# Performance work log

Hardware: AMD Instinct MI355X
Metric: run time of the kernel (lower is better)

## Reference

```python
import jax, jax.numpy as jnp
import numpy as np

N_NODES = 50000
N_EDGES = 800000
IN_CH = 128
OUT_CH = 64
BN_EPS = 1e-5


def setup_inputs() -> dict:
    key = jax.random.key(0)
    k1, k2, k3 = jax.random.split(key, 3)
    x = jax.random.normal(k1, (N_NODES, IN_CH), dtype=jnp.float32)
    edge_index = jax.random.randint(k2, (2, N_EDGES), 0, N_NODES, dtype=jnp.int64)
    W = jax.random.normal(k3, (IN_CH, OUT_CH), dtype=jnp.float32) / np.sqrt(IN_CH)
    bias = jnp.zeros((OUT_CH,), dtype=jnp.float32)
    gamma = jnp.ones((OUT_CH,), dtype=jnp.float32)
    beta = jnp.zeros((OUT_CH,), dtype=jnp.float32)
    return {"x": x, "edge_index": edge_index, "W": W, "bias": bias,
            "gamma": gamma, "beta": beta}


def reference(x, edge_index, W, bias, gamma, beta):
    N = x.shape[0]
    # Linear transform first (GCNConv order): [N, out]
    h = x @ W
    # Add self-loops
    loops = jnp.arange(N, dtype=edge_index.dtype)
    src = jnp.concatenate([edge_index[0], loops])  # [E+N]
    dst = jnp.concatenate([edge_index[1], loops])
    # Symmetric GCN normalization: deg^{-1/2}[src] * deg^{-1/2}[dst]
    ones = jnp.ones(dst.shape[0], dtype=h.dtype)
    deg = jax.ops.segment_sum(ones, dst, num_segments=N)
    dinv = jnp.where(deg > 0, jax.lax.rsqrt(deg), 0.0)
    norm = dinv[src] * dinv[dst]  # [E+N]
    # Gather, scale, scatter-add
    msgs = h[src] * norm[:, None]  # [E+N, out]
    agg = jax.ops.segment_sum(msgs, dst, num_segments=N) + bias  # [N, out]
    # tanh activation
    a = jnp.tanh(agg)
    # BatchNorm over node dim (training mode, biased var)
    mean = jnp.mean(a, axis=0)
    var = jnp.mean(jnp.square(a - mean), axis=0)
    return gamma * (a - mean) * jax.lax.rsqrt(var + BN_EPS) + beta
```

## Files before the change

kernel.cpp:

```cpp
#include <hip/hip_runtime.h>
#include <hip/hip_bf16.h>
#include <math.h>

#define N_NODES 50000
#define N_EDGES 800000
#define IN_CH 128
#define OUT_CH 64
#define BN_EPS 1e-5f
#define CAP 64

typedef __attribute__((ext_vector_type(8))) short short8;
typedef __attribute__((ext_vector_type(4))) float f32x4;

__device__ __forceinline__ float bf16u_to_f32(uint u) { return __uint_as_float(u << 16); }

__device__ __forceinline__ ushort f32_to_bf16(float f) {
    uint u = __float_as_uint(f);
    uint r = (u + 0x7fff + ((u >> 16) & 1)) >> 16;
    return (ushort)r;
}

__global__ void fill_slots_kernel(const int2* __restrict__ esrc2, const int2* __restrict__ edst2,
                                  int* __restrict__ cnt, ushort* __restrict__ slot, int E2) {
    int i = blockIdx.x * blockDim.x + threadIdx.x;
    if (i < E2) {
        int2 s = esrc2[i];
        int2 d = edst2[i];
        int p0 = atomicAdd(&cnt[d.x], 1);
        int p1 = atomicAdd(&cnt[d.y], 1);
        if (p0 < CAP) slot[d.x * CAP + p0] = (ushort)s.x;
        if (p1 < CAP) slot[d.y * CAP + p1] = (ushort)s.y;
    }
}

#define XPAD 136
__global__ __launch_bounds__(256) void gemm_mfma_kernel(const float* __restrict__ x,
                                                        const float* __restrict__ W,
                                                        const int* __restrict__ cnt,
                                                        ushort* __restrict__ hb,
                                                        float* __restrict__ dinv, int N) {
    __shared__ ushort xs[64 * XPAD];
    __shared__ ushort wt[64 * XPAD];
    int t = threadIdx.x;
    int lane = t & 63;
    int w = t >> 6;
    int nn = lane & 15;
    int quad = lane >> 4;
    int row0 = blockIdx.x * 64;

    const float4* W4 = (const float4*)W;
#pragma unroll
    for (int i = 0; i < 8; ++i) {
        int f4 = t + 256 * i;
        float4 v = W4[f4];
        int e0 = f4 * 4;
        int k = e0 >> 6;
        int n = e0 & 63;
        wt[(n + 0) * XPAD + k] = f32_to_bf16(v.x);
        wt[(n + 1) * XPAD + k] = f32_to_bf16(v.y);
        wt[(n + 2) * XPAD + k] = f32_to_bf16(v.z);
        wt[(n + 3) * XPAD + k] = f32_to_bf16(v.w);
    }
#pragma unroll
    for (int i = 0; i < 8; ++i) {
        int linear4 = t + 256 * i;
        int r = linear4 >> 5;
        int c4 = linear4 & 31;
        int gr = row0 + r; if (gr >= N) gr = N - 1;
        float4 v = *(const float4*)(x + (size_t)gr * IN_CH + c4 * 4);
        ushort u0 = f32_to_bf16(v.x), u1 = f32_to_bf16(v.y);
        ushort u2 = f32_to_bf16(v.z), u3 = f32_to_bf16(v.w);
        uint2 packed = make_uint2((uint)u0 | ((uint)u1 << 16), (uint)u2 | ((uint)u3 << 16));
        *(uint2*)&xs[r * XPAD + c4 * 4] = packed;
    }
    __syncthreads();

    short8 bfrag[4][4];
#pragma unroll
    for (int t2 = 0; t2 < 4; ++t2)
#pragma unroll
        for (int c = 0; c < 4; ++c)
            bfrag[t2][c] = *(const short8*)&wt[(16 * t2 + nn) * XPAD + 32 * c + quad * 8];

    f32x4 acc[4] = {{0.f, 0.f, 0.f, 0.f}, {0.f, 0.f, 0.f, 0.f},
                    {0.f, 0.f, 0.f, 0.f}, {0.f, 0.f, 0.f, 0.f}};
#pragma unroll
    for (int c = 0; c < 4; ++c) {
        short8 afrag = *(const short8*)&xs[(16 * w + nn) * XPAD + 32 * c + quad * 8];
#pragma unroll
        for (int t2 = 0; t2 < 4; ++t2)
            acc[t2] = __builtin_amdgcn_mfma_f32_16x16x32_bf16(afrag, bfrag[t2][c], acc[t2], 0, 0, 0);
    }

    int rbase = row0 + 16 * w + quad * 4;
    float dv[4];
#pragma unroll
    for (int r = 0; r < 4; ++r)
        dv[r] = (rbase + r < N) ? rsqrtf((float)(cnt[rbase + r] + 1)) : 0.f;
    if (nn == 0) {
#pragma unroll
        for (int r = 0; r < 4; ++r)
            if (rbase + r < N) dinv[rbase + r] = dv[r];
    }
#pragma unroll
    for (int t2 = 0; t2 < 4; ++t2) {
#pragma unroll
        for (int r = 0; r < 4; ++r) {
            int row = rbase + r;
            if (row < N) hb[(size_t)row * OUT_CH + 16 * t2 + nn] = f32_to_bf16(acc[t2][r] * dv[r]);
        }
    }
}

__device__ __forceinline__ float reduce_groups(float a0, float a1, float a2, float a3,
                                               float a4, float a5, float a6, float a7, int g) {
    float s0 = a0 + __shfl_xor(a0, 8);
    float s1 = a1 + __shfl_xor(a1, 8);
    float s2 = a2 + __shfl_xor(a2, 8);
    float s3 = a3 + __shfl_xor(a3, 8);
    float s4 = a4 + __shfl_xor(a4, 8);
    float s5 = a5 + __shfl_xor(a5, 8);
    float s6 = a6 + __shfl_xor(a6, 8);
    float s7 = a7 + __shfl_xor(a7, 8);
    bool h1 = (g & 1);
    float b0 = h1 ? s4 : s0, b1 = h1 ? s5 : s1, b2 = h1 ? s6 : s2, b3 = h1 ? s7 : s3;
    float u0 = b0 + __shfl_xor(b0, 16);
    float u1 = b1 + __shfl_xor(b1, 16);
    float u2 = b2 + __shfl_xor(b2, 16);
    float u3 = b3 + __shfl_xor(b3, 16);
    bool h2 = (g & 2);
    float c0 = h2 ? u2 : u0, c1 = h2 ? u3 : u1;
    float v0 = c0 + __shfl_xor(c0, 32);
    float v1 = c1 + __shfl_xor(c1, 32);
    return (g & 4) ? v1 : v0;
}

__global__ __launch_bounds__(256) void gather_fused_kernel(const int* __restrict__ cnt,
                                                           const ushort* __restrict__ slot,
                                                           const float* __restrict__ dinv,
                                                           const ushort* __restrict__ hb,
                                                           const float* __restrict__ bias,
                                                           float* __restrict__ out,
                                                           float* __restrict__ sums, int N) {
    int t = threadIdx.x;
    int lane = t & 63;
    int g = lane >> 3;
    int sub = lane & 7;
    int cidx = 8 * sub + (((g & 1) << 2) | (g & 2) | ((g >> 2) & 1));
    int wid = (blockIdx.x * blockDim.x + t) >> 6;
    int nw = (gridDim.x * blockDim.x) >> 6;
    float bias_c = bias[cidx];
    float ssum = 0.f, ssq = 0.f;

#define ISSUE(SV, MM, DN, J, H0, H1) do {                                  \
        int e0 = (J) + g, e1 = e0 + 8;                                     \
        int i0 = e0 - 1; i0 = (i0 < 0) ? 0 : i0;                           \
        int s0 = __shfl(SV, i0);                                           \
        int s1 = __shfl(SV, e1 - 1);                                       \
        s0 = (e0 == 0) ? (DN) : s0;                                        \
        s0 = (e0 < (MM)) ? s0 : N_NODES;                                   \
        s1 = (e1 < (MM)) ? s1 : N_NODES;                                   \
        H0 = *(const uint4*)(hb + ((size_t)s0 << 6) + (sub << 3));         \
        H1 = *(const uint4*)(hb + ((size_t)s1 << 6) + (sub << 3));         \
    } while (0)

#define CONS_A(H)                                                           \
        aA0 += __uint_as_float((H).x << 16); aA1 += __uint_as_float((H).x & 0xffff0000u); \
        aA2 += __uint_as_float((H).y << 16); aA3 += __uint_as_float((H).y & 0xffff0000u); \
        aA4 += __uint_as_float((H).z << 16); aA5 += __uint_as_float((H).z & 0xffff0000u); \
        aA6 += __uint_as_float((H).w << 16); aA7 += __uint_as_float((H).w & 0xffff0000u);

#define CONS_B(H)                                                           \
        aB0 += __uint_as_float((H).x << 16); aB1 += __uint_as_float((H).x & 0xffff0000u); \
        aB2 += __uint_as_float((H).y << 16); aB3 += __uint_as_float((H).y & 0xffff0000u); \
        aB4 += __uint_as_float((H).z << 16); aB5 += __uint_as_float((H).z & 0xffff0000u); \
        aB6 += __uint_as_float((H).w << 16); aB7 += __uint_as_float((H).w & 0xffff0000u);

    for (int dA = wid; dA < N; dA += 2 * nw) {
        int dB = dA + nw;
        bool hasB = dB < N;
        int dBc = hasB ? dB : dA;

        float ddA = dinv[dA];
        float ddB = dinv[dBc];
        int mA = cnt[dA]; if (mA > CAP) mA = CAP;
        int mB = cnt[dBc]; if (mB > CAP) mB = CAP;
        int svA = __builtin_nontemporal_load(&slot[(size_t)dA * CAP + lane]);
        int svB = __builtin_nontemporal_load(&slot[(size_t)dBc * CAP + lane]);
        int MA = mA + 1;
        int MB = hasB ? mB + 1 : 0;
        int Mmax = (MA > MB) ? MA : MB;

        float aA0 = 0.f, aA1 = 0.f, aA2 = 0.f, aA3 = 0.f;
        float aA4 = 0.f, aA5 = 0.f, aA6 = 0.f, aA7 = 0.f;
        float aB0 = 0.f, aB1 = 0.f, aB2 = 0.f, aB3 = 0.f;
        float aB4 = 0.f, aB5 = 0.f, aB6 = 0.f, aB7 = 0.f;

        uint4 hA0, hA1, hB0, hB1;
        ISSUE(svA, MA, dA, 0, hA0, hA1);
        ISSUE(svB, MB, dBc, 0, hB0, hB1);
        for (int j = 16; j < Mmax; j += 16) {
            uint4 nA0, nA1, nB0, nB1;
            ISSUE(svA, MA, dA, j, nA0, nA1);
            ISSUE(svB, MB, dBc, j, nB0, nB1);
            CONS_A(hA0); CONS_A(hA1);
            CONS_B(hB0); CONS_B(hB1);
            hA0 = nA0; hA1 = nA1; hB0 = nB0; hB1 = nB1;
        }
        CONS_A(hA0); CONS_A(hA1);
        CONS_B(hB0); CONS_B(hB1);

        float totalA = reduce_groups(aA0, aA1, aA2, aA3, aA4, aA5, aA6, aA7, g);
        float totalB = reduce_groups(aB0, aB1, aB2, aB3, aB4, aB5, aB6, aB7, g);

        float vA = tanhf(fmaf(ddA, totalA, bias_c));
        out[(size_t)dA * OUT_CH + cidx] = vA;
        ssum += vA;
        ssq += vA * vA;
        if (hasB) {
            float vB = tanhf(fmaf(ddB, totalB, bias_c));
            out[(size_t)dB * OUT_CH + cidx] = vB;
            ssum += vB;
            ssq += vB * vB;
        }
    }
#undef ISSUE
#undef CONS_A
#undef CONS_B

    __shared__ float ls[256];
    __shared__ float ls2[256];
    ls[t] = ssum; ls2[t] = ssq;
    __syncthreads();
    if (t < 128) { ls[t] += ls[t + 128]; ls2[t] += ls2[t + 128]; }
    __syncthreads();
    if (t < 64) {
        atomicAdd(&sums[cidx], ls[t] + ls[t + 64]);
        atomicAdd(&sums[64 + cidx], ls2[t] + ls2[t + 64]);
    }
}

__global__ __launch_bounds__(256) void bn_apply_kernel(float4* __restrict__ a,
                                                       const float* __restrict__ sums,
                                                       const float* __restrict__ gamma,
                                                       const float* __restrict__ beta, int total4) {
    int c0 = (threadIdx.x * 4) & 63;
    const float invN = 1.0f / (float)N_NODES;
    float4 scale, shift;
    {
        float m0 = sums[c0 + 0] * invN, m1 = sums[c0 + 1] * invN;
        float m2 = sums[c0 + 2] * invN, m3 = sums[c0 + 3] * invN;
        float v0 = sums[64 + c0 + 0] * invN - m0 * m0;
        float v1 = sums[64 + c0 + 1] * invN - m1 * m1;
        float v2 = sums[64 + c0 + 2] * invN - m2 * m2;
        float v3 = sums[64 + c0 + 3] * invN - m3 * m3;
        scale.x = gamma[c0 + 0] * rsqrtf(v0 + BN_EPS);
        scale.y = gamma[c0 + 1] * rsqrtf(v1 + BN_EPS);
        scale.z = gamma[c0 + 2] * rsqrtf(v2 + BN_EPS);
        scale.w = gamma[c0 + 3] * rsqrtf(v3 + BN_EPS);
        shift.x = beta[c0 + 0] - m0 * scale.x;
        shift.y = beta[c0 + 1] - m1 * scale.y;
        shift.z = beta[c0 + 2] - m2 * scale.z;
        shift.w = beta[c0 + 3] - m3 * scale.w;
    }
    int stride = gridDim.x * blockDim.x;
    for (int idx = blockIdx.x * blockDim.x + threadIdx.x; idx < total4; idx += stride) {
        float4 v = a[idx];
        v.x = v.x * scale.x + shift.x;
        v.y = v.y * scale.y + shift.y;
        v.z = v.z * scale.z + shift.z;
        v.w = v.w * scale.w + shift.w;
        a[idx] = v;
    }
}

extern "C" void kernel_launch(void* const* d_in, const int* in_sizes, int n_in,
                              void* d_out, int out_size, void* d_ws, size_t ws_size,
                              hipStream_t stream) {
    const float* x     = (const float*)d_in[0];
    const int*   eidx  = (const int*)d_in[1];
    const float* W     = (const float*)d_in[2];
    const float* bias  = (const float*)d_in[3];
    const float* gamma = (const float*)d_in[4];
    const float* beta  = (const float*)d_in[5];
    float* out = (float*)d_out;

    const int2* esrc2 = (const int2*)eidx;
    const int2* edst2 = (const int2*)(eidx + N_EDGES);

    ushort* hb   = (ushort*)d_ws;
    int*   cnt   = (int*)(hb + (size_t)(N_NODES + 1) * OUT_CH);
    float* sums  = (float*)(cnt + N_NODES);
    ushort* slot = (ushort*)(((uintptr_t)(sums + 128) + 255) & ~(uintptr_t)255);
    float* dinv  = (float*)(slot + (size_t)N_NODES * CAP);

    size_t zero_span = (size_t)OUT_CH * 2 + (size_t)N_NODES * 4 + 128 * 4;
    hipMemsetAsync(hb + (size_t)N_NODES * OUT_CH, 0, zero_span, stream);
    fill_slots_kernel<<<(N_EDGES / 2 + 255) / 256, 256, 0, stream>>>(esrc2, edst2, cnt, slot, N_EDGES / 2);
    gemm_mfma_kernel<<<(N_NODES + 63) / 64, 256, 0, stream>>>(x, W, cnt, hb, dinv, N_NODES);
    gather_fused_kernel<<<2048, 256, 0, stream>>>(cnt, slot, dinv, hb, bias, out, sums, N_NODES);
    bn_apply_kernel<<<512, 256, 0, stream>>>((float4*)out, sums, gamma, beta, N_NODES * OUT_CH / 4);
}
```

Before: 200.9 us.

## Assign contiguous node ranges per wave and prefetch slot lists up front

Each wave now owns a contiguous block of destination nodes instead of a grid-strided set. All slot indices for those nodes are loaded with four dwordx1 loads at kernel start, and their counts and dinv values are loaded with one lane-spread load. Slots are then unpacked two per dword through shuffles, which removes per-iteration dependent metadata loads. The code hardcodes 6 or 7 nodes per wave (three pairs plus an optional single), so it is only correct when the grid size makes N/nw fall in that range.

After: 199.7 us. No clear change (-0.6%).

```diff
diff --git a/kernel.cpp b/kernel.cpp
--- a/kernel.cpp
+++ b/kernel.cpp
@@ -135,6 +135,11 @@
     return (g & 4) ? v1 : v0;
 }
 
+__device__ __forceinline__ int extract_slot(int svj, int half, int p) {
+    uint r = (uint)__shfl(svj, half + (p >> 1));
+    return (int)((r >> ((p & 1) * 16)) & 0xffffu);
+}
+
 __global__ __launch_bounds__(256) void gather_fused_kernel(const int* __restrict__ cnt,
                                                            const ushort* __restrict__ slot,
                                                            const float* __restrict__ dinv,
@@ -147,16 +152,30 @@
     int g = lane >> 3;
     int sub = lane & 7;
     int cidx = 8 * sub + (((g & 1) << 2) | (g & 2) | ((g >> 2) & 1));
-    int wid = (blockIdx.x * blockDim.x + t) >> 6;
+    int wv = (blockIdx.x * blockDim.x + t) >> 6;
     int nw = (gridDim.x * blockDim.x) >> 6;
     float bias_c = bias[cidx];
     float ssum = 0.f, ssq = 0.f;
 
-#define ISSUE(SV, MM, DN, J, H0, H1) do {                                  \
+    int RQ = N / nw;
+    int RR = N - RQ * nw;
+    int s = wv * RQ + (wv < RR ? wv : RR);
+    int c = RQ + (wv < RR ? 1 : 0);
+
+    const int* sdw = (const int*)slot + (size_t)s * 32;
+    int sv0 = __builtin_nontemporal_load(sdw + lane);
+    int sv1 = __builtin_nontemporal_load(sdw + 64 + lane);
+    int sv2 = __builtin_nontemporal_load(sdw + 128 + lane);
+    int sv3 = __builtin_nontemporal_load(sdw + 192 + lane);
+    int mi = s + (lane & 7); if (mi > N - 1) mi = N - 1;
+    int mAll = cnt[mi];
+    float dAll = dinv[mi];
+
+#define ISSUE_N(SVJ, HALF, DN, MM, J, H0, H1) do {                         \
         int e0 = (J) + g, e1 = e0 + 8;                                     \
-        int i0 = e0 - 1; i0 = (i0 < 0) ? 0 : i0;                           \
-        int s0 = __shfl(SV, i0);                                           \
-        int s1 = __shfl(SV, e1 - 1);                                       \
+        int p0 = e0 - 1; p0 = (p0 < 0) ? 0 : p0;                           \
+        int s0 = extract_slot(SVJ, HALF, p0);                              \
+        int s1 = extract_slot(SVJ, HALF, e1 - 1);                          \
         s0 = (e0 == 0) ? (DN) : s0;                                        \
         s0 = (e0 < (MM)) ? s0 : N_NODES;                                   \
         s1 = (e1 < (MM)) ? s1 : N_NODES;                                   \
@@ -176,57 +195,70 @@
         aB4 += __uint_as_float((H).z << 16); aB5 += __uint_as_float((H).z & 0xffff0000u); \
         aB6 += __uint_as_float((H).w << 16); aB7 += __uint_as_float((H).w & 0xffff0000u);
 
-    for (int dA = wid; dA < N; dA += 2 * nw) {
-        int dB = dA + nw;
-        bool hasB = dB < N;
-        int dBc = hasB ? dB : dA;
-
-        float ddA = dinv[dA];
-        float ddB = dinv[dBc];
-        int mA = cnt[dA]; if (mA > CAP) mA = CAP;
-        int mB = cnt[dBc]; if (mB > CAP) mB = CAP;
-        int svA = __builtin_nontemporal_load(&slot[(size_t)dA * CAP + lane]);
-        int svB = __builtin_nontemporal_load(&slot[(size_t)dBc * CAP + lane]);
-        int MA = mA + 1;
-        int MB = hasB ? mB + 1 : 0;
-        int Mmax = (MA > MB) ? MA : MB;
-
-        float aA0 = 0.f, aA1 = 0.f, aA2 = 0.f, aA3 = 0.f;
-        float aA4 = 0.f, aA5 = 0.f, aA6 = 0.f, aA7 = 0.f;
-        float aB0 = 0.f, aB1 = 0.f, aB2 = 0.f, aB3 = 0.f;
-        float aB4 = 0.f, aB5 = 0.f, aB6 = 0.f, aB7 = 0.f;
-
-        uint4 hA0, hA1, hB0, hB1;
-        ISSUE(svA, MA, dA, 0, hA0, hA1);
-        ISSUE(svB, MB, dBc, 0, hB0, hB1);
-        for (int j = 16; j < Mmax; j += 16) {
-            uint4 nA0, nA1, nB0, nB1;
-            ISSUE(svA, MA, dA, j, nA0, nA1);
-            ISSUE(svB, MB, dBc, j, nB0, nB1);
-            CONS_A(hA0); CONS_A(hA1);
-            CONS_B(hB0); CONS_B(hB1);
-            hA0 = nA0; hA1 = nA1; hB0 = nB0; hB1 = nB1;
-        }
-        CONS_A(hA0); CONS_A(hA1);
-        CONS_B(hB0); CONS_B(hB1);
-
-        float totalA = reduce_groups(aA0, aA1, aA2, aA3, aA4, aA5, aA6, aA7, g);
-        float totalB = reduce_groups(aB0, aB1, aB2, aB3, aB4, aB5, aB6, aB7, g);
-
-        float vA = tanhf(fmaf(ddA, totalA, bias_c));
-        out[(size_t)dA * OUT_CH + cidx] = vA;
-        ssum += vA;
-        ssq += vA * vA;
-        if (hasB) {
-            float vB = tanhf(fmaf(ddB, totalB, bias_c));
-            out[(size_t)dB * OUT_CH + cidx] = vB;
-            ssum += vB;
-            ssq += vB * vB;
-        }
-    }
-#undef ISSUE
+#define PAIR(K, SVJ) do {                                                   \
+        int dA = s + (K);                                                   \
+        int dB = dA + 1;                                                    \
+        int mA = __shfl(mAll, (K));     if (mA > CAP) mA = CAP;             \
+        int mB = __shfl(mAll, (K) + 1); if (mB > CAP) mB = CAP;             \
+        float ddA = __shfl(dAll, (K));                                      \
+        float ddB = __shfl(dAll, (K) + 1);                                  \
+        int MA = mA + 1, MB = mB + 1;                                       \
+        int Mmax = (MA > MB) ? MA : MB;                                     \
+        float aA0=0.f,aA1=0.f,aA2=0.f,aA3=0.f,aA4=0.f,aA5=0.f,aA6=0.f,aA7=0.f; \
+        float aB0=0.f,aB1=0.f,aB2=0.f,aB3=0.f,aB4=0.f,aB5=0.f,aB6=0.f,aB7=0.f; \
+        uint4 hA0, hA1, hB0, hB1;                                           \
+        ISSUE_N(SVJ, 0,  dA, MA, 0, hA0, hA1);                              \
+        ISSUE_N(SVJ, 32, dB, MB, 0, hB0, hB1);                              \
+        for (int j = 16; j < Mmax; j += 16) {                               \
+            uint4 nA0, nA1, nB0, nB1;                                       \
+            ISSUE_N(SVJ, 0,  dA, MA, j, nA0, nA1);                          \
+            ISSUE_N(SVJ, 32, dB, MB, j, nB0, nB1);                          \
+            CONS_A(hA0); CONS_A(hA1); CONS_B(hB0); CONS_B(hB1);             \
+            hA0 = nA0; hA1 = nA1; hB0 = nB0; hB1 = nB1;                     \
+        }                                                                    \
+        CONS_A(hA0); CONS_A(hA1); CONS_B(hB0); CONS_B(hB1);                 \
+        float totalA = reduce_groups(aA0,aA1,aA2,aA3,aA4,aA5,aA6,aA7, g);   \
+        float totalB = reduce_groups(aB0,aB1,aB2,aB3,aB4,aB5,aB6,aB7, g);   \
+        float vA = tanhf(fmaf(ddA, totalA, bias_c));                        \
+        float vB = tanhf(fmaf(ddB, totalB, bias_c));                        \
+        out[(size_t)dA * OUT_CH + cidx] = vA;                               \
+        out[(size_t)dB * OUT_CH + cidx] = vB;                               \
+        ssum += vA + vB;                                                    \
+        ssq += vA * vA + vB * vB;                                           \
+    } while (0)
+
+#define SINGLE(K, SVJ) do {                                                 \
+        int dA = s + (K);                                                   \
+        int mA = __shfl(mAll, (K)); if (mA > CAP) mA = CAP;                 \
+        float ddA = __shfl(dAll, (K));                                      \
+        int MA = mA + 1;                                                    \
+        float aA0=0.f,aA1=0.f,aA2=0.f,aA3=0.f,aA4=0.f,aA5=0.f,aA6=0.f,aA7=0.f; \
+        uint4 hA0, hA1;                                                     \
+        ISSUE_N(SVJ, 0, dA, MA, 0, hA0, hA1);                               \
+        for (int j = 16; j < MA; j += 16) {                                 \
+            uint4 nA0, nA1;                                                 \
+            ISSUE_N(SVJ, 0, dA, MA, j, nA0, nA1);                           \
+            CONS_A(hA0); CONS_A(hA1);                                       \
+            hA0 = nA0; hA1 = nA1;                                           \
+        }                                                                    \
+        CONS_A(hA0); CONS_A(hA1);                                           \
+        float totalA = reduce_groups(aA0,aA1,aA2,aA3,aA4,aA5,aA6,aA7, g);   \
+        float vA = tanhf(fmaf(ddA, totalA, bias_c));                        \
+        out[(size_t)dA * OUT_CH + cidx] = vA;                               \
+        ssum += vA;                                                         \
+        ssq += vA * vA;                                                     \
+    } while (0)
+
+    PAIR(0, sv0);
+    PAIR(2, sv1);
+    PAIR(4, sv2);
+    if (c == 7) { SINGLE(6, sv3); }
+
+#undef ISSUE_N
 #undef CONS_A
 #undef CONS_B
+#undef PAIR
+#undef SINGLE
 
     __shared__ float ls[256];
     __shared__ float ls2[256];
```
